# Performance work log

Measured on AMD Instinct MI355X. Metric: run time of the kernel, lower is better.

The kernel has to match this reference:

```python
import jax, jax.numpy as jnp
import numpy as np

N, V, F, H, B, HID = 256, 32, 128, 8, 8, 64
R_MAX = 5.0
DH = F // H


def fc_edges(n):
    a = np.arange(n)
    s, r = np.meshgrid(a, a, indexing="ij")
    m = s != r
    return jnp.asarray(s[m]), jnp.asarray(r[m])

SENDERS, RECEIVERS = fc_edges(N)
E = N * (N - 1)


def sph_harmonics(u):
    # u: [..., 3] unit vectors -> [..., 15] = l=1(3)+l=2(5)+l=3(7), e3nn 'component' normalization
    x, y, z = u[..., 0], u[..., 1], u[..., 2]
    s3 = 3.0 ** 0.5; s5 = 5.0 ** 0.5; s7 = 7.0 ** 0.5
    s15 = 15.0 ** 0.5; s105 = 105.0 ** 0.5
    s35_8 = (35.0 / 8.0) ** 0.5; s21_8 = (21.0 / 8.0) ** 0.5
    l1 = [s3 * y, s3 * z, s3 * x]
    l2 = [s15 * x * y, s15 * y * z, 0.5 * s5 * (3 * z * z - 1),
          s15 * x * z, 0.5 * s15 * (x * x - y * y)]
    l3 = [s35_8 * y * (3 * x * x - y * y), s105 * x * y * z,
          s21_8 * y * (5 * z * z - 1), 0.5 * s7 * z * (5 * z * z - 3),
          s21_8 * x * (5 * z * z - 1), 0.5 * s105 * z * (x * x - y * y),
          s35_8 * x * (x * x - 3 * y * y)]
    return jnp.stack(l1 + l2 + l3, axis=-1)


def radial_embed(lengths):
    # Bessel basis (e3nn.bessel) times soft envelope (e3nn.soft_envelope)
    x = jnp.maximum(lengths, 1e-6)[..., None]
    k = jnp.arange(1, B + 1, dtype=lengths.dtype)
    bes = (2.0 / R_MAX) ** 0.5 * jnp.sin(k * jnp.pi * x / R_MAX) / x
    def sus(t):
        return jnp.where(t > 0, jnp.exp(-1.0 / jnp.where(t > 0, t, 1.0)), 0.0)
    env = 1.2 * sus(2.0 * (1.0 - lengths / R_MAX)) / sus(jnp.asarray(2.0))
    return bes * env[..., None]


def setup_inputs():
    key = jax.random.key(0)
    ks = jax.random.split(key, 16)
    def w(k, shape):
        return jax.random.normal(k, shape, jnp.float32) / (shape[0] ** 0.5)
    D_edge = 2 * F + V * B
    return {
        "positions": jax.random.normal(ks[0], (N, V, 3), jnp.float32),
        "features": jax.random.normal(ks[1], (N, F), jnp.float32),
        "We1": w(ks[2], (D_edge, HID)), "be1": jnp.zeros((HID,), jnp.float32),
        "We2": w(ks[3], (HID, HID)), "be2": jnp.zeros((HID,), jnp.float32),
        "W_q": w(ks[4], (F, F)), "W_k": w(ks[5], (HID, F)),
        "W_v": w(ks[6], (F, F)), "W_vec": w(ks[7], (HID, V)),
        "W_mix": w(ks[8], (V, V)),
        "M1": w(ks[9], (F, HID)), "bm1": jnp.zeros((HID,), jnp.float32),
        "M2": w(ks[10], (HID, HID)), "bm2": jnp.zeros((HID,), jnp.float32),
        "M3": w(ks[11], (HID, F)), "bm3": jnp.zeros((F,), jnp.float32),
    }


def reference(positions, features, We1, be1, We2, be2, W_q, W_k, W_v, W_vec,
              W_mix, M1, bm1, M2, bm2, M3, bm3):
    act = jax.nn.selu
    s, r = SENDERS, RECEIVERS
    vectors = positions[s] - positions[r]                        # [E, V, 3]
    lengths = jnp.sqrt(jnp.sum(vectors * vectors, -1) + 1e-18)   # [E, V] safe_norm
    unit = vectors / lengths[..., None]
    sph = sph_harmonics(unit)                                    # [E, V, 15]
    radial = radial_embed(lengths).reshape(E, V * B)             # [E, V*B]
    edge_weight_cutoff = jnp.ones((E,), positions.dtype)

    # edge MLP on invariants (radial embedding + src/dst scalar features)
    edge_in = jnp.concatenate([features[s], features[r], radial], -1)
    h = act(edge_in @ We1 + be1)
    h = act(h @ We2 + be2)                                       # [E, HID]

    # multi-head attention over incoming edges per node (segment softmax)
    q = (features @ W_q).reshape(N, H, DH)
    k = (h @ W_k).reshape(E, H, DH)
    logit = jnp.einsum("ehd,ehd->eh", k, q[r]) / (DH ** 0.5)
    lmax = jax.ops.segment_max(logit, r, num_segments=N)
    ex = edge_weight_cutoff[:, None] * jnp.exp(logit - lmax[r])
    denom = jax.ops.segment_sum(ex, r, num_segments=N)
    alpha = ex / (denom[r] + 1e-12)                              # [E, H]

    # invariant (0e) values
    v = (features[s] @ W_v).reshape(E, H, DH)
    inv_agg = jax.ops.segment_sum(alpha[..., None] * v, r, num_segments=N).reshape(N, F)

    # equivariant (1o) values: scalar-gated l=1 spherical harmonics (sqrt(3)*unit)
    coeff = h @ W_vec                                            # [E, V]
    alpha_v = jnp.repeat(alpha, V // H, axis=1)                  # [E, V]
    vec_msg = ((alpha_v * coeff) * (3.0 ** 0.5))[..., None] * unit  # [E, V, 3]
    vec_agg = jax.ops.segment_sum(vec_msg, r, num_segments=N)    # [N, V, 3]
    vec_out = jnp.einsum("nvc,vw->nwc", vec_agg, W_mix)

    # final invariant MLP + residuals
    hi = act(inv_agg @ M1 + bm1)
    hi = act(hi @ M2 + bm2)
    inv_out = hi @ M3 + bm3
    return (vec_out + positions, inv_out + features)
```

## Files before the change

kernel.cpp:

```cpp
#include <hip/hip_runtime.h>
#include <hip/hip_bf16.h>

#define NN 256
#define VC 32
#define FD 128

typedef unsigned int uint32;
typedef unsigned short u16;
typedef __attribute__((ext_vector_type(8))) short bf16x8;
typedef __attribute__((ext_vector_type(4))) float f32x4;

__device__ __forceinline__ float selu_f(float x) {
    const float lam = 1.0507009873554805f;
    const float la  = 1.7580993408473766f;
    return x > 0.f ? lam * x : la * (__expf(x) - 1.f);
}

__device__ __forceinline__ u16 f32_to_bf16_rne(float f) {
    uint32 u = __float_as_uint(f);
    uint32 r = (u + 0x7fffu + ((u >> 16) & 1u)) >> 16;
    return (u16)r;
}

__device__ __forceinline__ float bf16_to_f32(u16 h) {
    return __uint_as_float(((uint32)h) << 16);
}

__global__ __launch_bounds__(256) void k1_pre(
    const float* __restrict__ feat, const float* __restrict__ We1,
    const float* __restrict__ be1, const float* __restrict__ Wq,
    const float* __restrict__ Wk, const float* __restrict__ Wv,
    const float* __restrict__ Wvec, const float* __restrict__ We2,
    const float* __restrict__ pos,
    float* __restrict__ A, float* __restrict__ Bf, u16* __restrict__ kqb,
    u16* __restrict__ w1b, u16* __restrict__ we2b, u16* __restrict__ wvb,
    u16* __restrict__ fvtH, u16* __restrict__ fvtL,
    u16* __restrict__ ptH, u16* __restrict__ ptL,
    float* __restrict__ lgg2, u16* __restrict__ cfg2)
{
    __shared__ float fl[FD];
    __shared__ float ql[FD];
    const int n = blockIdx.x;
    const int t = threadIdx.x;
    {
        const int gid = n*256 + t;
        if (gid < 16384) {
            const int c = gid >> 8, k = gid & 255;
            w1b[gid] = f32_to_bf16_rne(We1[(256 + k)*64 + c]);
        } else if (gid < 20480) {
            const int o = gid - 16384;
            const int c = o >> 6, k = o & 63;
            we2b[o] = f32_to_bf16_rne(We2[k*64 + c]);
        } else if (gid < 22528) {
            const int o = gid - 20480;
            const int v = o >> 6, k = o & 63;
            wvb[o] = f32_to_bf16_rne(Wvec[k*32 + v]);
        }
    }
    if (t < FD) fl[t] = feat[n*FD + t];
    __syncthreads();
    if (t < 64) {
        float a = 0.f;
        for (int i = 0; i < FD; ++i) a = fmaf(fl[i], We1[i*64 + t], a);
        A[n*64 + t] = a;
    } else if (t < 128) {
        const int j = t - 64;
        float a = be1[j];
        for (int i = 0; i < FD; ++i) a = fmaf(fl[i], We1[(FD+i)*64 + j], a);
        Bf[n*64 + j] = a;
    } else {
        const int j = t - 128;
        float a = 0.f;
        for (int i = 0; i < FD; ++i) a = fmaf(fl[i], Wq[i*FD + j], a);
        ql[j] = a * 0.25f;
    }
    if (t < FD) {
        float a = 0.f;
        for (int i = 0; i < FD; ++i) a = fmaf(fl[i], Wv[i*FD + t], a);
        const u16 hi = f32_to_bf16_rne(a);
        const u16 lo = f32_to_bf16_rne(a - bf16_to_f32(hi));
        fvtH[t*256 + n] = hi;
        fvtL[t*256 + n] = lo;
    }
    if (t < 128) {
        const int v = t >> 2, c = t & 3;
        const float val = (c < 3) ? pos[(n*VC + v)*3 + c] : 1.0f;
        const u16 hi = f32_to_bf16_rne(val);
        const u16 lo = f32_to_bf16_rne(val - bf16_to_f32(hi));
        ptH[(v*4+c)*256 + n] = hi;
        ptL[(v*4+c)*256 + n] = lo;
    }
    if (t < 8)  lgg2[n*2048 + t*256 + n] = -1e30f;
    if (t < 32) cfg2[n*8192 + t*256 + n] = 0;
    __syncthreads();
    for (int o = t; o < 512; o += 256) {
        const int h = o >> 6, j = o & 63;
        float a = 0.f;
        #pragma unroll
        for (int d = 0; d < 16; ++d)
            a = fmaf(Wk[j*FD + h*16 + d], ql[h*16 + d], a);
        kqb[n*512 + o] = f32_to_bf16_rne(a);
    }
}

__global__ __launch_bounds__(256) void k2_edge(
    const float* __restrict__ pos, const float* __restrict__ be2,
    const float* __restrict__ Ag, const float* __restrict__ Bfg,
    const u16* __restrict__ w1b, const u16* __restrict__ we2b,
    const u16* __restrict__ wvb, const u16* __restrict__ kqb,
    float* __restrict__ lgg2, u16* __restrict__ cfg2)
{
    __shared__ u16 rad[8192];
    __shared__ u16 h1b[32*64];
    __shared__ u16 h2b[32*64];
    __shared__ float invl[32*33];

    const int t = threadIdx.x;
    const int wave = t >> 6, l = t & 63;
    const int li = l & 15, q = l >> 4;
    const int mh = wave >> 1, eh = wave & 1;
    const int r = blockIdx.x >> 2, part = blockIdx.x & 3;
    const int e = eh*16 + li;
    const int swz16 = (e & 7) << 3;

    bf16x8 w1A[2][8];
    #pragma unroll
    for (int mt = 0; mt < 2; ++mt) {
        const int c = mh*32 + mt*16 + li;
        #pragma unroll
        for (int kb = 0; kb < 8; ++kb)
            w1A[mt][kb] = *(const bf16x8*)(w1b + c*256 + kb*32 + q*8);
    }
    bf16x8 we2A[2][2];
    #pragma unroll
    for (int mt = 0; mt < 2; ++mt) {
        const int c2 = mh*32 + mt*16 + li;
        #pragma unroll
        for (int kb = 0; kb < 2; ++kb)
            we2A[mt][kb] = *(const bf16x8*)(we2b + c2*64 + kb*32 + q*8);
    }
    bf16x8 wvA[2];
    {
        const int v = mh*16 + li;
        #pragma unroll
        for (int kb = 0; kb < 2; ++kb)
            wvA[kb] = *(const bf16x8*)(wvb + v*64 + kb*32 + q*8);
    }
    bf16x8 kqA[2];
    if (li < 8) {
        #pragma unroll
        for (int kb = 0; kb < 2; ++kb)
            kqA[kb] = *(const bf16x8*)(kqb + r*512 + li*64 + kb*32 + q*8);
    } else {
        #pragma unroll
        for (int kb = 0; kb < 2; ++kb)
            #pragma unroll
            for (int j = 0; j < 8; ++j) kqA[kb][j] = 0;
    }
    float bfreg[2][4], be2reg[2][4];
    #pragma unroll
    for (int mt = 0; mt < 2; ++mt)
        #pragma unroll
        for (int rg = 0; rg < 4; ++rg) {
            const int c = mh*32 + mt*16 + q*4 + rg;
            bfreg[mt][rg] = Bfg[r*64 + c];
            be2reg[mt][rg] = be2[c];
        }

    for (int it = 0; it < 2; ++it) {
        const int s0 = (part*2 + it) * 32;
        const int sp = s0 + e;
        int s = sp + (sp >= r ? 1 : 0); if (s > 255) s = 255;
        __syncthreads();

        float As[2][4];
        #pragma unroll
        for (int mt = 0; mt < 2; ++mt)
            #pragma unroll
            for (int rg = 0; rg < 4; ++rg)
                As[mt][rg] = Ag[s*64 + mh*32 + mt*16 + q*4 + rg];

        {
            const int ep = t & 31, vg = t >> 5;
            const int spp = s0 + ep;
            int sv = spp + (spp >= r ? 1 : 0); if (sv > 255) sv = 255;
            #pragma unroll
            for (int kk = 0; kk < 4; ++kk) {
                const int v = vg*4 + kk;
                const float* ps = pos + (sv*VC + v)*3;
                const float* pr = pos + (r*VC + v)*3;
                const float dx = ps[0]-pr[0], dy = ps[1]-pr[1], dz = ps[2]-pr[2];
                const float d2 = fmaf(dx,dx,fmaf(dy,dy,dz*dz)) + 1e-18f;
                const float len = sqrtf(d2);
                invl[ep*33 + v] = rsqrtf(d2);
                const float x = fmaxf(len, 1e-6f);
                const float tt2 = 2.f - 0.4f*len;
                const float env = tt2 > 0.f ? 1.9784655248401538f * __expf(-1.f/tt2) : 0.f;
                const float coefc = 0.6324555320336759f * env / x;
                float s_cur, c1;
                __sincosf(0.6283185307179586f * x, &s_cur, &c1);
                const float c2x = 2.f * c1;
                float s_prev = 0.f;
                union { uint4 u4; u16 us[8]; } pk;
                #pragma unroll
                for (int b = 0; b < 8; ++b) {
                    pk.us[b] = f32_to_bf16_rne(coefc * s_cur);
                    const float s_next = fmaf(c2x, s_cur, -s_prev);
                    s_prev = s_cur; s_cur = s_next;
                }
                *(uint4*)((char*)rad + ((ep*512 + v*16) ^ ((ep & 15) << 4))) = pk.u4;
            }
        }
        __syncthreads();

        f32x4 d1[2] = {{0.f,0.f,0.f,0.f},{0.f,0.f,0.f,0.f}};
        #pragma unroll
        for (int kb = 0; kb < 8; ++kb) {
            const bf16x8 rf = *(const bf16x8*)((const char*)rad +
                                ((e*512 + (kb*4+q)*16) ^ ((e & 15) << 4)));
            d1[0] = __builtin_amdgcn_mfma_f32_16x16x32_bf16(w1A[0][kb], rf, d1[0], 0, 0, 0);
            d1[1] = __builtin_amdgcn_mfma_f32_16x16x32_bf16(w1A[1][kb], rf, d1[1], 0, 0, 0);
        }
        #pragma unroll
        for (int mt = 0; mt < 2; ++mt) {
            const int c0 = mh*32 + mt*16 + q*4;
            const u16 p0 = f32_to_bf16_rne(selu_f(d1[mt][0] + As[mt][0] + bfreg[mt][0]));
            const u16 p1 = f32_to_bf16_rne(selu_f(d1[mt][1] + As[mt][1] + bfreg[mt][1]));
            const u16 p2 = f32_to_bf16_rne(selu_f(d1[mt][2] + As[mt][2] + bfreg[mt][2]));
            const u16 p3 = f32_to_bf16_rne(selu_f(d1[mt][3] + As[mt][3] + bfreg[mt][3]));
            *(uint32*)&h1b[e*64 + ((c0)     ^ swz16)] = (uint32)p0 | ((uint32)p1 << 16);
            *(uint32*)&h1b[e*64 + ((c0 + 2) ^ swz16)] = (uint32)p2 | ((uint32)p3 << 16);
        }
        __syncthreads();

        f32x4 d2[2] = {{0.f,0.f,0.f,0.f},{0.f,0.f,0.f,0.f}};
        #pragma unroll
        for (int kb = 0; kb < 2; ++kb) {
            const bf16x8 hb = *(const bf16x8*)&h1b[e*64 + ((kb*32 + q*8) ^ swz16)];
            d2[0] = __builtin_amdgcn_mfma_f32_16x16x32_bf16(we2A[0][kb], hb, d2[0], 0, 0, 0);
            d2[1] = __builtin_amdgcn_mfma_f32_16x16x32_bf16(we2A[1][kb], hb, d2[1], 0, 0, 0);
        }
        #pragma unroll
        for (int mt = 0; mt < 2; ++mt) {
            const int c0 = mh*32 + mt*16 + q*4;
            const u16 p0 = f32_to_bf16_rne(selu_f(d2[mt][0] + be2reg[mt][0]));
            const u16 p1 = f32_to_bf16_rne(selu_f(d2[mt][1] + be2reg[mt][1]));
            const u16 p2 = f32_to_bf16_rne(selu_f(d2[mt][2] + be2reg[mt][2]));
            const u16 p3 = f32_to_bf16_rne(selu_f(d2[mt][3] + be2reg[mt][3]));
            *(uint32*)&h2b[e*64 + ((c0)     ^ swz16)] = (uint32)p0 | ((uint32)p1 << 16);
            *(uint32*)&h2b[e*64 + ((c0 + 2) ^ swz16)] = (uint32)p2 | ((uint32)p3 << 16);
        }
        __syncthreads();

        f32x4 d3 = {0.f,0.f,0.f,0.f};
        f32x4 dl = {0.f,0.f,0.f,0.f};
        #pragma unroll
        for (int kb = 0; kb < 2; ++kb) {
            const bf16x8 hb = *(const bf16x8*)&h2b[e*64 + ((kb*32 + q*8) ^ swz16)];
            d3 = __builtin_amdgcn_mfma_f32_16x16x32_bf16(wvA[kb], hb, d3, 0, 0, 0);
            if (mh == 0)
                dl = __builtin_amdgcn_mfma_f32_16x16x32_bf16(kqA[kb], hb, dl, 0, 0, 0);
        }
        if (sp < 255) {
            #pragma unroll
            for (int rg = 0; rg < 4; ++rg) {
                const int v = mh*16 + q*4 + rg;
                cfg2[(size_t)r*8192 + v*256 + s] =
                    f32_to_bf16_rne(d3[rg] * 1.7320508075688772f * invl[e*33 + v]);
            }
            if (mh == 0 && q < 2) {
                #pragma unroll
                for (int rg = 0; rg < 4; ++rg)
                    lgg2[(size_t)r*2048 + (q*4+rg)*256 + s] = dl[rg];
            }
        }
    }
}

__global__ __launch_bounds__(64) void k3b_agg(
    const float* __restrict__ lgg2, const u16* __restrict__ cfg2,
    const u16* __restrict__ fvtH, const u16* __restrict__ fvtL,
    const u16* __restrict__ ptH, const u16* __restrict__ ptL,
    float* __restrict__ inv, float* __restrict__ vec4)
{
    const int l = threadIdx.x, li = l & 15, q = l >> 4;
    const int b = blockIdx.x;
    if (b < 128) {
        const int h = b >> 4, r0 = (b & 15) * 16;
        bf16x8 fH[8], fL[8];
        #pragma unroll
        for (int kb = 0; kb < 8; ++kb) {
            fH[kb] = *(const bf16x8*)(fvtH + (h*16+li)*256 + kb*32 + q*8);
            fL[kb] = *(const bf16x8*)(fvtL + (h*16+li)*256 + kb*32 + q*8);
        }
        const float* lgr = lgg2 + (size_t)(r0+li)*2048 + h*256;
        float mx = -3.0e38f;
        #pragma unroll
        for (int kb = 0; kb < 8; ++kb) {
            const float4 g0 = *(const float4*)(lgr + kb*32 + q*8);
            const float4 g1 = *(const float4*)(lgr + kb*32 + q*8 + 4);
            mx = fmaxf(mx, fmaxf(fmaxf(g0.x,g0.y), fmaxf(g0.z,g0.w)));
            mx = fmaxf(mx, fmaxf(fmaxf(g1.x,g1.y), fmaxf(g1.z,g1.w)));
        }
        mx = fmaxf(mx, __shfl_xor(mx, 16));
        mx = fmaxf(mx, __shfl_xor(mx, 32));
        float sm = 0.f;
        f32x4 Ch = {0.f,0.f,0.f,0.f};
        f32x4 Cl = {0.f,0.f,0.f,0.f};
        #pragma unroll
        for (int kb = 0; kb < 8; ++kb) {
            const float4 g0 = *(const float4*)(lgr + kb*32 + q*8);
            const float4 g1 = *(const float4*)(lgr + kb*32 + q*8 + 4);
            float ev[8];
            ev[0]=__expf(g0.x-mx); ev[1]=__expf(g0.y-mx); ev[2]=__expf(g0.z-mx); ev[3]=__expf(g0.w-mx);
            ev[4]=__expf(g1.x-mx); ev[5]=__expf(g1.y-mx); ev[6]=__expf(g1.z-mx); ev[7]=__expf(g1.w-mx);
            bf16x8 a;
            #pragma unroll
            for (int j = 0; j < 8; ++j) { sm += ev[j]; a[j] = (short)f32_to_bf16_rne(ev[j]); }
            Ch = __builtin_amdgcn_mfma_f32_16x16x32_bf16(a, fH[kb], Ch, 0, 0, 0);
            Cl = __builtin_amdgcn_mfma_f32_16x16x32_bf16(a, fL[kb], Cl, 0, 0, 0);
        }
        sm += __shfl_xor(sm, 16);
        sm += __shfl_xor(sm, 32);
        #pragma unroll
        for (int rg = 0; rg < 4; ++rg) {
            const float d = __shfl(sm, q*4 + rg);
            inv[(r0 + q*4 + rg)*128 + h*16 + li] = (Ch[rg] + Cl[rg]) / (d + 1e-12f);
        }
    } else {
        const int b2 = b - 128, v = b2 >> 4, r0 = (b2 & 15) * 16;
        const int h = v >> 2;
        bf16x8 pH[8], pL[8];
        #pragma unroll
        for (int kb = 0; kb < 8; ++kb) {
            if (li < 4) {
                pH[kb] = *(const bf16x8*)(ptH + (v*4+li)*256 + kb*32 + q*8);
                pL[kb] = *(const bf16x8*)(ptL + (v*4+li)*256 + kb*32 + q*8);
            } else {
                #pragma unroll
                for (int j = 0; j < 8; ++j) { pH[kb][j] = 0; pL[kb][j] = 0; }
            }
        }
        const float* lgr = lgg2 + (size_t)(r0+li)*2048 + h*256;
        const u16*  cfr = cfg2 + (size_t)(r0+li)*8192 + v*256;
        float mx = -3.0e38f;
        #pragma unroll
        for (int kb = 0; kb < 8; ++kb) {
            const float4 g0 = *(const float4*)(lgr + kb*32 + q*8);
            const float4 g1 = *(const float4*)(lgr + kb*32 + q*8 + 4);
            mx = fmaxf(mx, fmaxf(fmaxf(g0.x,g0.y), fmaxf(g0.z,g0.w)));
            mx = fmaxf(mx, fmaxf(fmaxf(g1.x,g1.y), fmaxf(g1.z,g1.w)));
        }
        mx = fmaxf(mx, __shfl_xor(mx, 16));
        mx = fmaxf(mx, __shfl_xor(mx, 32));
        float sm = 0.f;
        f32x4 Ch = {0.f,0.f,0.f,0.f};
        f32x4 Cl = {0.f,0.f,0.f,0.f};
        #pragma unroll
        for (int kb = 0; kb < 8; ++kb) {
            const float4 g0 = *(const float4*)(lgr + kb*32 + q*8);
            const float4 g1 = *(const float4*)(lgr + kb*32 + q*8 + 4);
            const bf16x8 cf8 = *(const bf16x8*)(cfr + kb*32 + q*8);
            float ev[8];
            ev[0]=__expf(g0.x-mx); ev[1]=__expf(g0.y-mx); ev[2]=__expf(g0.z-mx); ev[3]=__expf(g0.w-mx);
            ev[4]=__expf(g1.x-mx); ev[5]=__expf(g1.y-mx); ev[6]=__expf(g1.z-mx); ev[7]=__expf(g1.w-mx);
            bf16x8 a;
            #pragma unroll
            for (int j = 0; j < 8; ++j) {
                sm += ev[j];
                a[j] = (short)f32_to_bf16_rne(ev[j] * bf16_to_f32((u16)cf8[j]));
            }
            Ch = __builtin_amdgcn_mfma_f32_16x16x32_bf16(a, pH[kb], Ch, 0, 0, 0);
            Cl = __builtin_amdgcn_mfma_f32_16x16x32_bf16(a, pL[kb], Cl, 0, 0, 0);
        }
        sm += __shfl_xor(sm, 16);
        sm += __shfl_xor(sm, 32);
        #pragma unroll
        for (int rg = 0; rg < 4; ++rg) {
            const float d = __shfl(sm, q*4 + rg);
            if (li < 4)
                vec4[(r0 + q*4 + rg)*128 + v*4 + li] = (Ch[rg] + Cl[rg]) / (d + 1e-12f);
        }
    }
}

__global__ __launch_bounds__(64) void k3c_out(
    const float* __restrict__ pos, const float* __restrict__ feat,
    const float* __restrict__ inv, const float* __restrict__ vec4,
    const float* __restrict__ Wmix,
    const float* __restrict__ M1, const float* __restrict__ bm1,
    const float* __restrict__ M2, const float* __restrict__ bm2,
    const float* __restrict__ M3, const float* __restrict__ bm3,
    float* __restrict__ out0, float* __restrict__ out1)
{
    __shared__ float inva[128];
    __shared__ float vec4s[128];
    __shared__ float pos96[96];
    __shared__ float vecl[96];
    __shared__ float hi1[64];
    __shared__ float hi2[64];
    const int r = blockIdx.x;
    const int l = threadIdx.x;
    inva[l]       = inv[r*128 + l];
    inva[64 + l]  = inv[r*128 + 64 + l];
    vec4s[l]      = vec4[r*128 + l];
    vec4s[64 + l] = vec4[r*128 + 64 + l];
    for (int o = l; o < 96; o += 64) pos96[o] = pos[r*96 + o];
    __syncthreads();
    for (int o = l; o < 96; o += 64) {
        const int v = o / 3, c = o - v*3;
        vecl[o] = vec4s[v*4 + c] - vec4s[v*4 + 3] * pos96[o];
    }
    float a1 = bm1[l];
    #pragma unroll 8
    for (int k = 0; k < 128; ++k) a1 = fmaf(inva[k], M1[k*64 + l], a1);
    hi1[l] = selu_f(a1);
    __syncthreads();
    float a2 = bm2[l];
    #pragma unroll 8
    for (int k = 0; k < 64; ++k) a2 = fmaf(hi1[k], M2[k*64 + l], a2);
    hi2[l] = selu_f(a2);
    __syncthreads();
    #pragma unroll
    for (int o0 = 0; o0 < 128; o0 += 64) {
        const int o = o0 + l;
        float a = bm3[o];
        #pragma unroll 8
        for (int k = 0; k < 64; ++k) a = fmaf(hi2[k], M3[k*128 + o], a);
        out1[r*128 + o] = a + feat[r*128 + o];
    }
    for (int o = l; o < 96; o += 64) {
        const int w = o / 3, c = o - w*3;
        float a = 0.f;
        #pragma unroll
        for (int v = 0; v < 32; ++v)
            a = fmaf(vecl[v*3 + c], Wmix[v*32 + w], a);
        out0[r*96 + o] = a + pos96[o];
    }
}

extern "C" void kernel_launch(void* const* d_in, const int* in_sizes, int n_in,
                              void* d_out, int out_size, void* d_ws, size_t ws_size,
                              hipStream_t stream)
{
    const float* pos  = (const float*)d_in[0];
    const float* feat = (const float*)d_in[1];
    const float* We1  = (const float*)d_in[2];
    const float* be1  = (const float*)d_in[3];
    const float* We2  = (const float*)d_in[4];
    const float* be2  = (const float*)d_in[5];
    const float* Wq   = (const float*)d_in[6];
    const float* Wk   = (const float*)d_in[7];
    const float* Wv   = (const float*)d_in[8];
    const float* Wvec = (const float*)d_in[9];
    const float* Wmix = (const float*)d_in[10];
    const float* M1   = (const float*)d_in[11];
    const float* bm1  = (const float*)d_in[12];
    const float* M2   = (const float*)d_in[13];
    const float* bm2  = (const float*)d_in[14];
    const float* M3   = (const float*)d_in[15];
    const float* bm3  = (const float*)d_in[16];

    char* ws = (char*)d_ws;
    float* A    = (float*)(ws + 0);
    float* Bf   = (float*)(ws + 65536);
    u16*   kqb  = (u16*)(ws + 131072);
    u16*   w1b  = (u16*)(ws + 393216);
    u16*   we2b = (u16*)(ws + 425984);
    u16*   wvb  = (u16*)(ws + 434176);
    u16*   fvtH = (u16*)(ws + 438272);
    u16*   fvtL = (u16*)(ws + 503808);
    u16*   ptH  = (u16*)(ws + 569344);
    u16*   ptL  = (u16*)(ws + 634880);
    float* lgg2 = (float*)(ws + 700416);
    u16*   cfg2 = (u16*)(ws + 2797568);
    float* inv   = (float*)(ws + 0);
    float* vec4  = (float*)(ws + 131072);
    if (ws_size < (size_t)6991872) return;

    float* out0 = (float*)d_out;
    float* out1 = out0 + NN*VC*3;

    hipLaunchKernelGGL(k1_pre, dim3(256), dim3(256), 0, stream,
                       feat, We1, be1, Wq, Wk, Wv, Wvec, We2, pos,
                       A, Bf, kqb, w1b, we2b, wvb, fvtH, fvtL, ptH, ptL, lgg2, cfg2);
    hipLaunchKernelGGL(k2_edge, dim3(1024), dim3(256), 0, stream,
                       pos, be2, A, Bf, w1b, we2b, wvb, kqb, lgg2, cfg2);
    hipLaunchKernelGGL(k3b_agg, dim3(640), dim3(64), 0, stream,
                       lgg2, cfg2, fvtH, fvtL, ptH, ptL, inv, vec4);
    hipLaunchKernelGGL(k3c_out, dim3(256), dim3(64), 0, stream,
                       pos, feat, inv, vec4, Wmix,
                       M1, bm1, M2, bm2, M3, bm3, out0, out1);
}
```

Baseline: 53.73 us.

## Rebalance work across kernels: split k1 blocks, fewer edge blocks, wider output kernel

The preprocessing kernel's 256 blocks become 512: the Wv projection and the position hi/lo splitting move into a second set of blocks, which shortens the serial work per block. The edge kernel now runs 512 blocks, each handling 4 sender tiles instead of 2, so the register-resident weight loads are amortised over more edges at the cost of fewer blocks in flight. The output kernel grows from 64 to 256 threads: the M1 reduction is split four ways and the M3 and Wmix outputs are computed in parallel. All arguments are passed as one Params struct, which is a refactor with no intended speed effect.

```diff
diff --git a/kernel.cpp b/kernel.cpp
--- a/kernel.cpp
+++ b/kernel.cpp
@@ -26,100 +26,101 @@
     return __uint_as_float(((uint32)h) << 16);
 }
 
-__global__ __launch_bounds__(256) void k1_pre(
-    const float* __restrict__ feat, const float* __restrict__ We1,
-    const float* __restrict__ be1, const float* __restrict__ Wq,
-    const float* __restrict__ Wk, const float* __restrict__ Wv,
-    const float* __restrict__ Wvec, const float* __restrict__ We2,
-    const float* __restrict__ pos,
-    float* __restrict__ A, float* __restrict__ Bf, u16* __restrict__ kqb,
-    u16* __restrict__ w1b, u16* __restrict__ we2b, u16* __restrict__ wvb,
-    u16* __restrict__ fvtH, u16* __restrict__ fvtL,
-    u16* __restrict__ ptH, u16* __restrict__ ptL,
-    float* __restrict__ lgg2, u16* __restrict__ cfg2)
+struct Params {
+    const float *pos, *feat, *We1, *be1, *We2, *be2, *Wq, *Wk, *Wv, *Wvec,
+                *Wmix, *M1, *bm1, *M2, *bm2, *M3, *bm3;
+    float *A, *Bf;
+    u16 *kqb, *w1b, *we2b, *wvb, *fvtH, *fvtL, *ptH, *ptL;
+    float *lgg2;
+    u16 *cfg2;
+    float *inv, *vec4;
+    float *out0, *out1;
+};
+
+__global__ __launch_bounds__(256) void k1_pre(Params P)
 {
     __shared__ float fl[FD];
     __shared__ float ql[FD];
-    const int n = blockIdx.x;
+    const int vb = blockIdx.x;
     const int t = threadIdx.x;
-    {
-        const int gid = n*256 + t;
-        if (gid < 16384) {
-            const int c = gid >> 8, k = gid & 255;
-            w1b[gid] = f32_to_bf16_rne(We1[(256 + k)*64 + c]);
-        } else if (gid < 20480) {
-            const int o = gid - 16384;
-            const int c = o >> 6, k = o & 63;
-            we2b[o] = f32_to_bf16_rne(We2[k*64 + c]);
-        } else if (gid < 22528) {
-            const int o = gid - 20480;
-            const int v = o >> 6, k = o & 63;
-            wvb[o] = f32_to_bf16_rne(Wvec[k*32 + v]);
-        }
-    }
-    if (t < FD) fl[t] = feat[n*FD + t];
-    __syncthreads();
-    if (t < 64) {
-        float a = 0.f;
-        for (int i = 0; i < FD; ++i) a = fmaf(fl[i], We1[i*64 + t], a);
-        A[n*64 + t] = a;
-    } else if (t < 128) {
-        const int j = t - 64;
-        float a = be1[j];
-        for (int i = 0; i < FD; ++i) a = fmaf(fl[i], We1[(FD+i)*64 + j], a);
-        Bf[n*64 + j] = a;
+    if (vb < 256) {
+        const int n = vb;
+        {
+            const int gid = n*256 + t;
+            if (gid < 16384) {
+                const int c = gid >> 8, k = gid & 255;
+                P.w1b[gid] = f32_to_bf16_rne(P.We1[(256 + k)*64 + c]);
+            } else if (gid < 20480) {
+                const int o = gid - 16384;
+                const int c = o >> 6, k = o & 63;
+                P.we2b[o] = f32_to_bf16_rne(P.We2[k*64 + c]);
+            } else if (gid < 22528) {
+                const int o = gid - 20480;
+                const int v = o >> 6, k = o & 63;
+                P.wvb[o] = f32_to_bf16_rne(P.Wvec[k*32 + v]);
+            }
+        }
+        if (t < FD) fl[t] = P.feat[n*FD + t];
+        __syncthreads();
+        if (t < 64) {
+            float a = 0.f;
+            for (int i = 0; i < FD; ++i) a = fmaf(fl[i], P.We1[i*64 + t], a);
+            P.A[n*64 + t] = a;
+        } else if (t < 128) {
+            const int j = t - 64;
+            float a = P.be1[j];
+            for (int i = 0; i < FD; ++i) a = fmaf(fl[i], P.We1[(FD+i)*64 + j], a);
+            P.Bf[n*64 + j] = a;
+        } else {
+            const int j = t - 128;
+            float a = 0.f;
+            for (int i = 0; i < FD; ++i) a = fmaf(fl[i], P.Wq[i*FD + j], a);
+            ql[j] = a * 0.25f;
+        }
+        if (t < 8)  P.lgg2[n*2048 + t*256 + n] = -1e30f;
+        if (t < 32) P.cfg2[(size_t)n*8192 + t*256 + n] = 0;
+        __syncthreads();
+        for (int o = t; o < 512; o += 256) {
+            const int h = o >> 6, j = o & 63;
+            float a = 0.f;
+            #pragma unroll
+            for (int d = 0; d < 16; ++d)
+                a = fmaf(P.Wk[j*FD + h*16 + d], ql[h*16 + d], a);
+            P.kqb[n*512 + o] = f32_to_bf16_rne(a);
+        }
     } else {
-        const int j = t - 128;
-        float a = 0.f;
-        for (int i = 0; i < FD; ++i) a = fmaf(fl[i], Wq[i*FD + j], a);
-        ql[j] = a * 0.25f;
-    }
-    if (t < FD) {
-        float a = 0.f;
-        for (int i = 0; i < FD; ++i) a = fmaf(fl[i], Wv[i*FD + t], a);
-        const u16 hi = f32_to_bf16_rne(a);
-        const u16 lo = f32_to_bf16_rne(a - bf16_to_f32(hi));
-        fvtH[t*256 + n] = hi;
-        fvtL[t*256 + n] = lo;
-    }
-    if (t < 128) {
-        const int v = t >> 2, c = t & 3;
-        const float val = (c < 3) ? pos[(n*VC + v)*3 + c] : 1.0f;
-        const u16 hi = f32_to_bf16_rne(val);
-        const u16 lo = f32_to_bf16_rne(val - bf16_to_f32(hi));
-        ptH[(v*4+c)*256 + n] = hi;
-        ptL[(v*4+c)*256 + n] = lo;
-    }
-    if (t < 8)  lgg2[n*2048 + t*256 + n] = -1e30f;
-    if (t < 32) cfg2[n*8192 + t*256 + n] = 0;
-    __syncthreads();
-    for (int o = t; o < 512; o += 256) {
-        const int h = o >> 6, j = o & 63;
-        float a = 0.f;
-        #pragma unroll
-        for (int d = 0; d < 16; ++d)
-            a = fmaf(Wk[j*FD + h*16 + d], ql[h*16 + d], a);
-        kqb[n*512 + o] = f32_to_bf16_rne(a);
-    }
-}
-
-__global__ __launch_bounds__(256) void k2_edge(
-    const float* __restrict__ pos, const float* __restrict__ be2,
-    const float* __restrict__ Ag, const float* __restrict__ Bfg,
-    const u16* __restrict__ w1b, const u16* __restrict__ we2b,
-    const u16* __restrict__ wvb, const u16* __restrict__ kqb,
-    float* __restrict__ lgg2, u16* __restrict__ cfg2)
+        const int n = vb - 256;
+        if (t < FD) fl[t] = P.feat[n*FD + t];
+        __syncthreads();
+        if (t < FD) {
+            float a = 0.f;
+            for (int i = 0; i < FD; ++i) a = fmaf(fl[i], P.Wv[i*FD + t], a);
+            const u16 hi = f32_to_bf16_rne(a);
+            const u16 lo = f32_to_bf16_rne(a - bf16_to_f32(hi));
+            P.fvtH[t*256 + n] = hi;
+            P.fvtL[t*256 + n] = lo;
+            const int v = t >> 2, c = t & 3;
+            const float val = (c < 3) ? P.pos[(n*VC + v)*3 + c] : 1.0f;
+            const u16 phi = f32_to_bf16_rne(val);
+            const u16 plo = f32_to_bf16_rne(val - bf16_to_f32(phi));
+            P.ptH[(v*4+c)*256 + n] = phi;
+            P.ptL[(v*4+c)*256 + n] = plo;
+        }
+    }
+}
+
+__global__ __launch_bounds__(256) void k2_edge(Params P)
 {
     __shared__ u16 rad[8192];
-    __shared__ u16 h1b[32*64];
-    __shared__ u16 h2b[32*64];
-    __shared__ float invl[32*33];
+    __shared__ u16 h1b[2048];
+    __shared__ u16 h2b[2048];
+    __shared__ float invl[1056];
 
     const int t = threadIdx.x;
     const int wave = t >> 6, l = t & 63;
     const int li = l & 15, q = l >> 4;
     const int mh = wave >> 1, eh = wave & 1;
-    const int r = blockIdx.x >> 2, part = blockIdx.x & 3;
+    const int r = blockIdx.x >> 1, tpart = blockIdx.x & 1;
     const int e = eh*16 + li;
     const int swz16 = (e & 7) << 3;
 
@@ -129,7 +130,7 @@
         const int c = mh*32 + mt*16 + li;
         #pragma unroll
         for (int kb = 0; kb < 8; ++kb)
-            w1A[mt][kb] = *(const bf16x8*)(w1b + c*256 + kb*32 + q*8);
+            w1A[mt][kb] = *(const bf16x8*)(P.w1b + c*256 + kb*32 + q*8);
     }
     bf16x8 we2A[2][2];
     #pragma unroll
@@ -137,20 +138,20 @@
         const int c2 = mh*32 + mt*16 + li;
         #pragma unroll
         for (int kb = 0; kb < 2; ++kb)
-            we2A[mt][kb] = *(const bf16x8*)(we2b + c2*64 + kb*32 + q*8);
+            we2A[mt][kb] = *(const bf16x8*)(P.we2b + c2*64 + kb*32 + q*8);
     }
     bf16x8 wvA[2];
     {
         const int v = mh*16 + li;
         #pragma unroll
         for (int kb = 0; kb < 2; ++kb)
-            wvA[kb] = *(const bf16x8*)(wvb + v*64 + kb*32 + q*8);
+            wvA[kb] = *(const bf16x8*)(P.wvb + v*64 + kb*32 + q*8);
     }
     bf16x8 kqA[2];
     if (li < 8) {
         #pragma unroll
         for (int kb = 0; kb < 2; ++kb)
-            kqA[kb] = *(const bf16x8*)(kqb + r*512 + li*64 + kb*32 + q*8);
+            kqA[kb] = *(const bf16x8*)(P.kqb + r*512 + li*64 + kb*32 + q*8);
     } else {
         #pragma unroll
         for (int kb = 0; kb < 2; ++kb)
@@ -163,12 +164,12 @@
         #pragma unroll
         for (int rg = 0; rg < 4; ++rg) {
             const int c = mh*32 + mt*16 + q*4 + rg;
-            bfreg[mt][rg] = Bfg[r*64 + c];
-            be2reg[mt][rg] = be2[c];
-        }
-
-    for (int it = 0; it < 2; ++it) {
-        const int s0 = (part*2 + it) * 32;
+            bfreg[mt][rg] = P.Bf[r*64 + c];
+            be2reg[mt][rg] = P.be2[c];
+        }
+
+    for (int it = 0; it < 4; ++it) {
+        const int s0 = (tpart*4 + it) * 32;
         const int sp = s0 + e;
         int s = sp + (sp >= r ? 1 : 0); if (s > 255) s = 255;
         __syncthreads();
@@ -178,7 +179,7 @@
         for (int mt = 0; mt < 2; ++mt)
             #pragma unroll
             for (int rg = 0; rg < 4; ++rg)
-                As[mt][rg] = Ag[s*64 + mh*32 + mt*16 + q*4 + rg];
+                As[mt][rg] = P.A[s*64 + mh*32 + mt*16 + q*4 + rg];
 
         {
             const int ep = t & 31, vg = t >> 5;
@@ -187,8 +188,8 @@
             #pragma unroll
             for (int kk = 0; kk < 4; ++kk) {
                 const int v = vg*4 + kk;
-                const float* ps = pos + (sv*VC + v)*3;
-                const float* pr = pos + (r*VC + v)*3;
+                const float* ps = P.pos + (sv*VC + v)*3;
+                const float* pr = P.pos + (r*VC + v)*3;
                 const float dx = ps[0]-pr[0], dy = ps[1]-pr[1], dz = ps[2]-pr[2];
                 const float d2 = fmaf(dx,dx,fmaf(dy,dy,dz*dz)) + 1e-18f;
                 const float len = sqrtf(d2);
@@ -203,8 +204,8 @@
                 float s_prev = 0.f;
                 union { uint4 u4; u16 us[8]; } pk;
                 #pragma unroll
-                for (int b = 0; b < 8; ++b) {
-                    pk.us[b] = f32_to_bf16_rne(coefc * s_cur);
+                for (int bb = 0; bb < 8; ++bb) {
+                    pk.us[bb] = f32_to_bf16_rne(coefc * s_cur);
                     const float s_next = fmaf(c2x, s_cur, -s_prev);
                     s_prev = s_cur; s_cur = s_next;
                 }
@@ -265,35 +266,31 @@
             #pragma unroll
             for (int rg = 0; rg < 4; ++rg) {
                 const int v = mh*16 + q*4 + rg;
-                cfg2[(size_t)r*8192 + v*256 + s] =
+                P.cfg2[(size_t)r*8192 + v*256 + s] =
                     f32_to_bf16_rne(d3[rg] * 1.7320508075688772f * invl[e*33 + v]);
             }
             if (mh == 0 && q < 2) {
                 #pragma unroll
                 for (int rg = 0; rg < 4; ++rg)
-                    lgg2[(size_t)r*2048 + (q*4+rg)*256 + s] = dl[rg];
-            }
-        }
-    }
-}
-
-__global__ __launch_bounds__(64) void k3b_agg(
-    const float* __restrict__ lgg2, const u16* __restrict__ cfg2,
-    const u16* __restrict__ fvtH, const u16* __restrict__ fvtL,
-    const u16* __restrict__ ptH, const u16* __restrict__ ptL,
-    float* __restrict__ inv, float* __restrict__ vec4)
+                    P.lgg2[(size_t)r*2048 + (q*4+rg)*256 + s] = dl[rg];
+            }
+        }
+    }
+}
+
+__global__ __launch_bounds__(64) void k3b_agg(Params P)
 {
     const int l = threadIdx.x, li = l & 15, q = l >> 4;
-    const int b = blockIdx.x;
-    if (b < 128) {
-        const int h = b >> 4, r0 = (b & 15) * 16;
+    const int task = blockIdx.x;
+    if (task < 128) {
+        const int h = task >> 4, r0 = (task & 15) * 16;
         bf16x8 fH[8], fL[8];
         #pragma unroll
         for (int kb = 0; kb < 8; ++kb) {
-            fH[kb] = *(const bf16x8*)(fvtH + (h*16+li)*256 + kb*32 + q*8);
-            fL[kb] = *(const bf16x8*)(fvtL + (h*16+li)*256 + kb*32 + q*8);
-        }
-        const float* lgr = lgg2 + (size_t)(r0+li)*2048 + h*256;
+            fH[kb] = *(const bf16x8*)(P.fvtH + (h*16+li)*256 + kb*32 + q*8);
+            fL[kb] = *(const bf16x8*)(P.fvtL + (h*16+li)*256 + kb*32 + q*8);
+        }
+        const float* lgr = P.lgg2 + (size_t)(r0+li)*2048 + h*256;
         float mx = -3.0e38f;
         #pragma unroll
         for (int kb = 0; kb < 8; ++kb) {
@@ -304,7 +301,7 @@
         }
         mx = fmaxf(mx, __shfl_xor(mx, 16));
         mx = fmaxf(mx, __shfl_xor(mx, 32));
-        float sm = 0.f;
+        float ssum = 0.f;
         f32x4 Ch = {0.f,0.f,0.f,0.f};
         f32x4 Cl = {0.f,0.f,0.f,0.f};
         #pragma unroll
@@ -316,33 +313,33 @@
             ev[4]=__expf(g1.x-mx); ev[5]=__expf(g1.y-mx); ev[6]=__expf(g1.z-mx); ev[7]=__expf(g1.w-mx);
             bf16x8 a;
             #pragma unroll
-            for (int j = 0; j < 8; ++j) { sm += ev[j]; a[j] = (short)f32_to_bf16_rne(ev[j]); }
+            for (int j = 0; j < 8; ++j) { ssum += ev[j]; a[j] = (short)f32_to_bf16_rne(ev[j]); }
             Ch = __builtin_amdgcn_mfma_f32_16x16x32_bf16(a, fH[kb], Ch, 0, 0, 0);
             Cl = __builtin_amdgcn_mfma_f32_16x16x32_bf16(a, fL[kb], Cl, 0, 0, 0);
         }
-        sm += __shfl_xor(sm, 16);
-        sm += __shfl_xor(sm, 32);
+        ssum += __shfl_xor(ssum, 16);
+        ssum += __shfl_xor(ssum, 32);
         #pragma unroll
         for (int rg = 0; rg < 4; ++rg) {
-            const float d = __shfl(sm, q*4 + rg);
-            inv[(r0 + q*4 + rg)*128 + h*16 + li] = (Ch[rg] + Cl[rg]) / (d + 1e-12f);
+            const float d = __shfl(ssum, q*4 + rg);
+            P.inv[(r0 + q*4 + rg)*128 + h*16 + li] = (Ch[rg] + Cl[rg]) / (d + 1e-12f);
         }
     } else {
-        const int b2 = b - 128, v = b2 >> 4, r0 = (b2 & 15) * 16;
+        const int b2 = task - 128, v = b2 >> 4, r0 = (b2 & 15) * 16;
         const int h = v >> 2;
         bf16x8 pH[8], pL[8];
         #pragma unroll
         for (int kb = 0; kb < 8; ++kb) {
             if (li < 4) {
-                pH[kb] = *(const bf16x8*)(ptH + (v*4+li)*256 + kb*32 + q*8);
-                pL[kb] = *(const bf16x8*)(ptL + (v*4+li)*256 + kb*32 + q*8);
+                pH[kb] = *(const bf16x8*)(P.ptH + (v*4+li)*256 + kb*32 + q*8);
+                pL[kb] = *(const bf16x8*)(P.ptL + (v*4+li)*256 + kb*32 + q*8);
             } else {
                 #pragma unroll
                 for (int j = 0; j < 8; ++j) { pH[kb][j] = 0; pL[kb][j] = 0; }
             }
         }
-        const float* lgr = lgg2 + (size_t)(r0+li)*2048 + h*256;
-        const u16*  cfr = cfg2 + (size_t)(r0+li)*8192 + v*256;
+        const float* lgr = P.lgg2 + (size_t)(r0+li)*2048 + h*256;
+        const u16*  cfr = P.cfg2 + (size_t)(r0+li)*8192 + v*256;
         float mx = -3.0e38f;
         #pragma unroll
         for (int kb = 0; kb < 8; ++kb) {
@@ -353,7 +350,7 @@
         }
         mx = fmaxf(mx, __shfl_xor(mx, 16));
         mx = fmaxf(mx, __shfl_xor(mx, 32));
-        float sm = 0.f;
+        float ssum = 0.f;
         f32x4 Ch = {0.f,0.f,0.f,0.f};
         f32x4 Cl = {0.f,0.f,0.f,0.f};
         #pragma unroll
@@ -367,32 +364,26 @@
             bf16x8 a;
             #pragma unroll
             for (int j = 0; j < 8; ++j) {
-                sm += ev[j];
+                ssum += ev[j];
                 a[j] = (short)f32_to_bf16_rne(ev[j] * bf16_to_f32((u16)cf8[j]));
             }
             Ch = __builtin_amdgcn_mfma_f32_16x16x32_bf16(a, pH[kb], Ch, 0, 0, 0);
             Cl = __builtin_amdgcn_mfma_f32_16x16x32_bf16(a, pL[kb], Cl, 0, 0, 0);
         }
-        sm += __shfl_xor(sm, 16);
-        sm += __shfl_xor(sm, 32);
+        ssum += __shfl_xor(ssum, 16);
+        ssum += __shfl_xor(ssum, 32);
         #pragma unroll
         for (int rg = 0; rg < 4; ++rg) {
-            const float d = __shfl(sm, q*4 + rg);
+            const float d = __shfl(ssum, q*4 + rg);
             if (li < 4)
-                vec4[(r0 + q*4 + rg)*128 + v*4 + li] = (Ch[rg] + Cl[rg]) / (d + 1e-12f);
-        }
-    }
-}
-
-__global__ __launch_bounds__(64) void k3c_out(
-    const float* __restrict__ pos, const float* __restrict__ feat,
-    const float* __restrict__ inv, const float* __restrict__ vec4,
-    const float* __restrict__ Wmix,
-    const float* __restrict__ M1, const float* __restrict__ bm1,
-    const float* __restrict__ M2, const float* __restrict__ bm2,
-    const float* __restrict__ M3, const float* __restrict__ bm3,
-    float* __restrict__ out0, float* __restrict__ out1)
+                P.vec4[(r0 + q*4 + rg)*128 + v*4 + li] = (Ch[rg] + Cl[rg]) / (d + 1e-12f);
+        }
+    }
+}
+
+__global__ __launch_bounds__(256) void k3c_out(Params P)
 {
+    __shared__ float part[4][64];
     __shared__ float inva[128];
     __shared__ float vec4s[128];
     __shared__ float pos96[96];
@@ -400,42 +391,50 @@
     __shared__ float hi1[64];
     __shared__ float hi2[64];
     const int r = blockIdx.x;
-    const int l = threadIdx.x;
-    inva[l]       = inv[r*128 + l];
-    inva[64 + l]  = inv[r*128 + 64 + l];
-    vec4s[l]      = vec4[r*128 + l];
-    vec4s[64 + l] = vec4[r*128 + 64 + l];
-    for (int o = l; o < 96; o += 64) pos96[o] = pos[r*96 + o];
+    const int t = threadIdx.x;
+    if (t < 128) inva[t] = P.inv[r*128 + t];
+    else         vec4s[t-128] = P.vec4[r*128 + (t-128)];
+    if (t < 96)  pos96[t] = P.pos[r*96 + t];
     __syncthreads();
-    for (int o = l; o < 96; o += 64) {
-        const int v = o / 3, c = o - v*3;
-        vecl[o] = vec4s[v*4 + c] - vec4s[v*4 + 3] * pos96[o];
-    }
-    float a1 = bm1[l];
-    #pragma unroll 8
-    for (int k = 0; k < 128; ++k) a1 = fmaf(inva[k], M1[k*64 + l], a1);
-    hi1[l] = selu_f(a1);
+    if (t < 96) {
+        const int v = t / 3, c = t - v*3;
+        vecl[t] = vec4s[v*4 + c] - vec4s[v*4 + 3] * pos96[t];
+    }
+    {
+        const int f = t & 63, g = t >> 6;
+        const int k0 = g*32;
+        float acc = 0.f;
+        #pragma unroll 8
+        for (int k = k0; k < k0 + 32; ++k)
+            acc = fmaf(inva[k], P.M1[k*64 + f], acc);
+        part[g][f] = acc;
+    }
     __syncthreads();
-    float a2 = bm2[l];
-    #pragma unroll 8
-    for (int k = 0; k < 64; ++k) a2 = fmaf(hi1[k], M2[k*64 + l], a2);
-    hi2[l] = selu_f(a2);
+    if (t < 64) {
+        const float a1 = P.bm1[t] + part[0][t] + part[1][t] + part[2][t] + part[3][t];
+        hi1[t] = selu_f(a1);
+    }
     __syncthreads();
-    #pragma unroll
-    for (int o0 = 0; o0 < 128; o0 += 64) {
-        const int o = o0 + l;
-        float a = bm3[o];
+    if (t < 64) {
+        float a2 = P.bm2[t];
         #pragma unroll 8
-        for (int k = 0; k < 64; ++k) a = fmaf(hi2[k], M3[k*128 + o], a);
-        out1[r*128 + o] = a + feat[r*128 + o];
-    }
-    for (int o = l; o < 96; o += 64) {
+        for (int k = 0; k < 64; ++k) a2 = fmaf(hi1[k], P.M2[k*64 + t], a2);
+        hi2[t] = selu_f(a2);
+    }
+    __syncthreads();
+    if (t < 128) {
+        float a = P.bm3[t];
+        #pragma unroll 8
+        for (int k = 0; k < 64; ++k) a = fmaf(hi2[k], P.M3[k*128 + t], a);
+        P.out1[r*128 + t] = a + P.feat[r*128 + t];
+    } else if (t < 224) {
+        const int o = t - 128;
         const int w = o / 3, c = o - w*3;
         float a = 0.f;
         #pragma unroll
         for (int v = 0; v < 32; ++v)
-            a = fmaf(vecl[v*3 + c], Wmix[v*32 + w], a);
-        out0[r*96 + o] = a + pos96[o];
+            a = fmaf(vecl[v*3 + c], P.Wmix[v*32 + w], a);
+        P.out0[r*96 + o] = a + pos96[o];
     }
 }
 
@@ -443,52 +442,48 @@
                               void* d_out, int out_size, void* d_ws, size_t ws_size,
                               hipStream_t stream)
 {
-    const float* pos  = (const float*)d_in[0];
-    const float* feat = (const float*)d_in[1];
-    const float* We1  = (const float*)d_in[2];
-    const float* be1  = (const float*)d_in[3];
-    const float* We2  = (const float*)d_in[4];
-    const float* be2  = (const float*)d_in[5];
-    const float* Wq   = (const float*)d_in[6];
-    const float* Wk   = (const float*)d_in[7];
-    const float* Wv   = (const float*)d_in[8];
-    const float* Wvec = (const float*)d_in[9];
-    const float* Wmix = (const float*)d_in[10];
-    const float* M1   = (const float*)d_in[11];
-    const float* bm1  = (const float*)d_in[12];
-    const float* M2   = (const float*)d_in[13];
-    const float* bm2  = (const float*)d_in[14];
-    const float* M3   = (const float*)d_in[15];
-    const float* bm3  = (const float*)d_in[16];
-
     char* ws = (char*)d_ws;
-    float* A    = (float*)(ws + 0);
-    float* Bf   = (float*)(ws + 65536);
-    u16*   kqb  = (u16*)(ws + 131072);
-    u16*   w1b  = (u16*)(ws + 393216);
-    u16*   we2b = (u16*)(ws + 425984);
-    u16*   wvb  = (u16*)(ws + 434176);
-    u16*   fvtH = (u16*)(ws + 438272);
-    u16*   fvtL = (u16*)(ws + 503808);
-    u16*   ptH  = (u16*)(ws + 569344);
-    u16*   ptL  = (u16*)(ws + 634880);
-    float* lgg2 = (float*)(ws + 700416);
-    u16*   cfg2 = (u16*)(ws + 2797568);
-    float* inv   = (float*)(ws + 0);
-    float* vec4  = (float*)(ws + 131072);
     if (ws_size < (size_t)6991872) return;
 
-    float* out0 = (float*)d_out;
-    float* out1 = out0 + NN*VC*3;
-
-    hipLaunchKernelGGL(k1_pre, dim3(256), dim3(256), 0, stream,
-                       feat, We1, be1, Wq, Wk, Wv, Wvec, We2, pos,
-                       A, Bf, kqb, w1b, we2b, wvb, fvtH, fvtL, ptH, ptL, lgg2, cfg2);
-    hipLaunchKernelGGL(k2_edge, dim3(1024), dim3(256), 0, stream,
-                       pos, be2, A, Bf, w1b, we2b, wvb, kqb, lgg2, cfg2);
-    hipLaunchKernelGGL(k3b_agg, dim3(640), dim3(64), 0, stream,
-                       lgg2, cfg2, fvtH, fvtL, ptH, ptL, inv, vec4);
-    hipLaunchKernelGGL(k3c_out, dim3(256), dim3(64), 0, stream,
-                       pos, feat, inv, vec4, Wmix,
-                       M1, bm1, M2, bm2, M3, bm3, out0, out1);
-}
+    Params p;
+    p.pos  = (const float*)d_in[0];
+    p.feat = (const float*)d_in[1];
+    p.We1  = (const float*)d_in[2];
+    p.be1  = (const float*)d_in[3];
+    p.We2  = (const float*)d_in[4];
+    p.be2  = (const float*)d_in[5];
+    p.Wq   = (const float*)d_in[6];
+    p.Wk   = (const float*)d_in[7];
+    p.Wv   = (const float*)d_in[8];
+    p.Wvec = (const float*)d_in[9];
+    p.Wmix = (const float*)d_in[10];
+    p.M1   = (const float*)d_in[11];
+    p.bm1  = (const float*)d_in[12];
+    p.M2   = (const float*)d_in[13];
+    p.bm2  = (const float*)d_in[14];
+    p.M3   = (const float*)d_in[15];
+    p.bm3  = (const float*)d_in[16];
+
+    p.A    = (float*)(ws + 0);
+    p.Bf   = (float*)(ws + 65536);
+    p.kqb  = (u16*)(ws + 131072);
+    p.w1b  = (u16*)(ws + 393216);
+    p.we2b = (u16*)(ws + 425984);
+    p.wvb  = (u16*)(ws + 434176);
+    p.fvtH = (u16*)(ws + 438272);
+    p.fvtL = (u16*)(ws + 503808);
+    p.ptH  = (u16*)(ws + 569344);
+    p.ptL  = (u16*)(ws + 634880);
+    p.lgg2 = (float*)(ws + 700416);
+    p.cfg2 = (u16*)(ws + 2797568);
+    p.inv  = (float*)(ws + 0);
+    p.vec4 = (float*)(ws + 131072);
+
+    p.out0 = (float*)d_out;
+    p.out1 = p.out0 + NN*VC*3;
+
+    hipLaunchKernelGGL(k1_pre,  dim3(512), dim3(256), 0, stream, p);
+    hipLaunchKernelGGL(k2_edge, dim3(512), dim3(256), 0, stream, p);
+    hipLaunchKernelGGL(k3b_agg, dim3(640), dim3(64),  0, stream, p);
+    hipLaunchKernelGGL(k3c_out, dim3(256), dim3(256), 0, stream, p);
+}
```

Result: faster. 44.56 us (-17.1%).
